# Kernel optimization log

Measured on AMD Instinct MI355X. Metric: run time of the kernel, lower is better.

## Reference

```python
import jax, jax.numpy as jnp
import numpy as np

D = 2048      # input_dim
E = 64        # num_experts
K = 2         # top-k
TEMP = 1.0    # temperature


def setup_inputs() -> dict:
    key = jax.random.key(0)
    ks = jax.random.split(key, 10)
    B, S = 4, 4096
    x = jax.random.normal(ks[0], (B, S, D), dtype=jnp.float32)
    u = jax.random.uniform(ks[1], (B, S, E), dtype=jnp.float32, minval=1e-7, maxval=1.0 - 1e-7)
    # Xavier-uniform init like the torch module (bias zeros)
    def xavier(k, fan_in, fan_out):
        lim = np.sqrt(6.0 / (fan_in + fan_out))
        return jax.random.uniform(k, (fan_in, fan_out), dtype=jnp.float32, minval=-lim, maxval=lim)
    return {
        "x": x, "u": u,
        "W1r": xavier(ks[2], D, D), "b1r": jnp.zeros((D,), jnp.float32),
        "W2r": xavier(ks[3], D, E), "b2r": jnp.zeros((E,), jnp.float32),
        "W1b": xavier(ks[4], D, D), "b1b": jnp.zeros((D,), jnp.float32),
        "W2b": xavier(ks[5], D, 1), "b2b": jnp.zeros((1,), jnp.float32),
    }


def reference(x, u, W1r, b1r, W2r, b2r, W1b, b1b, W2b, b2b):
    # Router MLP: Linear -> GELU(exact) -> Linear  (dropout=0)
    h_r = jax.nn.gelu(jnp.einsum("bsd,de->bse", x, W1r) + b1r, approximate=False)
    expert_scores = jnp.einsum("bsd,de->bse", h_r, W2r) + b2r            # [B,S,E]
    # Baseline MLP -> scalar per token
    h_b = jax.nn.gelu(jnp.einsum("bsd,de->bse", x, W1b) + b1b, approximate=False)
    baseline = (jnp.einsum("bsd,de->bse", h_b, W2b) + b2b)[..., 0]       # [B,S]
    # Training path: Gumbel noise + softmax + top-k (first softmax in torch src is dead code)
    gumbel = -jnp.log(-jnp.log(u))
    expert_probs = jax.nn.softmax((expert_scores + gumbel) / TEMP, axis=-1)
    expert_weights, expert_indices = jax.lax.top_k(expert_probs, K)      # [B,S,K]
    policy_gradient = jax.lax.stop_gradient(expert_weights - baseline[..., None])
    return expert_weights, expert_indices, baseline, policy_gradient, expert_scores
```

## Files before the change

### kernel.cpp

```cpp
#include <hip/hip_runtime.h>
#include <math.h>

#define D_IN   2048
#define E_NUM  64
#define NTOK   16384

#define BM     64
#define BN     256
#define BK     32
#define NTHR   256
#define LDA    68
#define LDH    68
#define NCHUNK (D_IN / BN)
#define NKITER (D_IN / BK)


__global__ __launch_bounds__(NTHR, 2)
void fused_mlp_kernel(const float* __restrict__ x,
                      const float* __restrict__ W1r, const float* __restrict__ b1r,
                      const float* __restrict__ W2r, const float* __restrict__ b2r,
                      const float* __restrict__ W1b, const float* __restrict__ b1b,
                      const float* __restrict__ W2b, const float* __restrict__ b2b,
                      float* __restrict__ out_scores,
                      float* __restrict__ out_baseline)
{
    extern __shared__ float smem[];
    float* As  = smem;
    float* Bs  = smem + BK * LDA;
    float* hsT = smem;

    const int tid    = threadIdx.x;
    const int isBase = blockIdx.y;
    const int row0   = blockIdx.x * BM;

    const float* W1 = isBase ? W1b : W1r;
    const float* b1 = isBase ? b1b : b1r;

    const int ty = tid >> 5;
    const int tx = tid & 31;

    const int sm  = tid >> 3;
    const int skq = tid & 7;
    const int bk4 = tid >> 6;
    const int bn4 = (tid & 63) * 4;

    const int sy = tid >> 4;
    const int sx = tid & 15;
    double acc2[4][4] = {};
    const int tb = tid & 63;
    const int hg = tid >> 6;
    double blacc = 0.0;

    for (int ch = 0; ch < NCHUNK; ++ch) {
        const int col0 = ch * BN;
        double acc[8][8] = {};

        for (int kc = 0; kc < NKITER; ++kc) {
            const int k0 = kc * BK;
            __syncthreads();

            const float* xp = x + (size_t)(row0 + sm) * D_IN + (k0 + 4 * skq);
            float4 xv0 = *(const float4*)xp;
            float4 xv1 = *(const float4*)(xp + (size_t)32 * D_IN);
            const float* wp = W1 + (size_t)(k0 + bk4) * D_IN + (col0 + bn4);
            float4 wv[8];
            #pragma unroll
            for (int j = 0; j < 8; ++j)
                wv[j] = *(const float4*)(wp + (size_t)(4 * j) * D_IN);

            As[(4 * skq + 0) * LDA + sm] = xv0.x;
            As[(4 * skq + 1) * LDA + sm] = xv0.y;
            As[(4 * skq + 2) * LDA + sm] = xv0.z;
            As[(4 * skq + 3) * LDA + sm] = xv0.w;
            As[(4 * skq + 0) * LDA + sm + 32] = xv1.x;
            As[(4 * skq + 1) * LDA + sm + 32] = xv1.y;
            As[(4 * skq + 2) * LDA + sm + 32] = xv1.z;
            As[(4 * skq + 3) * LDA + sm + 32] = xv1.w;
            #pragma unroll
            for (int j = 0; j < 8; ++j)
                *(float4*)&Bs[(bk4 + 4 * j) * BN + bn4] = wv[j];

            __syncthreads();

            #pragma unroll 4
            for (int kk = 0; kk < BK; ++kk) {
                float4 A0 = *(float4*)&As[kk * LDA + 8 * ty];
                float4 A1 = *(float4*)&As[kk * LDA + 8 * ty + 4];
                float4 B0 = *(float4*)&Bs[kk * BN + 4 * tx];
                float4 B1 = *(float4*)&Bs[kk * BN + 128 + 4 * tx];
                double a64[8] = {(double)A0.x, (double)A0.y, (double)A0.z, (double)A0.w,
                                 (double)A1.x, (double)A1.y, (double)A1.z, (double)A1.w};
                double b64[8] = {(double)B0.x, (double)B0.y, (double)B0.z, (double)B0.w,
                                 (double)B1.x, (double)B1.y, (double)B1.z, (double)B1.w};
                #pragma unroll
                for (int i = 0; i < 8; ++i)
                    #pragma unroll
                    for (int j = 0; j < 8; ++j)
                        acc[i][j] = fma(a64[i], b64[j], acc[i][j]);
            }
        }

        __syncthreads();
        #pragma unroll
        for (int j = 0; j < 8; ++j) {
            const int c = (j < 4) ? (4 * tx + j) : (128 + 4 * tx + (j - 4));
            const double bias = (double)b1[col0 + c];
            float h[8];
            #pragma unroll
            for (int i = 0; i < 8; ++i) {
                const double z = acc[i][j] + bias;
                h[i] = (float)(0.5 * z * (1.0 + erf(z * 0.70710678118654752440)));
            }
            *(float4*)&hsT[c * LDH + 8 * ty]     = make_float4(h[0], h[1], h[2], h[3]);
            *(float4*)&hsT[c * LDH + 8 * ty + 4] = make_float4(h[4], h[5], h[6], h[7]);
        }
        __syncthreads();

        if (!isBase) {
            #pragma unroll 2
            for (int hq = 0; hq < BN / 4; ++hq) {
                #pragma unroll
                for (int s = 0; s < 4; ++s) {
                    const int h = 4 * hq + s;
                    float4 A  = *(float4*)&hsT[h * LDH + 4 * sy];
                    float4 Bv = *(const float4*)&W2r[(size_t)(col0 + h) * E_NUM + 4 * sx];
                    double av[4] = {(double)A.x, (double)A.y, (double)A.z, (double)A.w};
                    double bv[4] = {(double)Bv.x, (double)Bv.y, (double)Bv.z, (double)Bv.w};
                    #pragma unroll
                    for (int r = 0; r < 4; ++r)
                        #pragma unroll
                        for (int e = 0; e < 4; ++e)
                            acc2[r][e] = fma(av[r], bv[e], acc2[r][e]);
                }
            }
        } else {
            #pragma unroll 4
            for (int hh = 0; hh < 64; ++hh) {
                const int h = hg * 64 + hh;
                blacc = fma((double)hsT[h * LDH + tb], (double)W2b[col0 + h], blacc);
            }
        }
    }

    __syncthreads();

    if (!isBase) {
        #pragma unroll
        for (int r = 0; r < 4; ++r) {
            float4 o;
            o.x = (float)(acc2[r][0] + (double)b2r[4 * sx + 0]);
            o.y = (float)(acc2[r][1] + (double)b2r[4 * sx + 1]);
            o.z = (float)(acc2[r][2] + (double)b2r[4 * sx + 2]);
            o.w = (float)(acc2[r][3] + (double)b2r[4 * sx + 3]);
            *(float4*)&out_scores[(size_t)(row0 + 4 * sy + r) * E_NUM + 4 * sx] = o;
        }
    } else {
        double* red = (double*)smem;
        red[tid] = blacc;
        __syncthreads();
        if (tid < 64) {
            double bl = red[tid] + red[64 + tid] + red[128 + tid] + red[192 + tid]
                      + (double)b2b[0];
            out_baseline[row0 + tid] = (float)bl;
        }
    }
}

__global__ __launch_bounds__(256)
void softmax_topk_kernel(const float* __restrict__ scores,
                         const float* __restrict__ u,
                         const float* __restrict__ baseline,
                         float* __restrict__ out_w,
                         float* __restrict__ out_i,
                         float* __restrict__ out_pg)
{
    const int tok  = (blockIdx.x * blockDim.x + threadIdx.x) >> 6;
    const int lane = threadIdx.x & 63;

    const double s  = (double)scores[(size_t)tok * E_NUM + lane];
    const double uu = (double)u[(size_t)tok * E_NUM + lane];
    const double g  = -log(-log(uu));
    const double v  = s + g;

    double m = v;
    #pragma unroll
    for (int off = 32; off > 0; off >>= 1)
        m = fmax(m, __shfl_xor(m, off, 64));
    const double p = exp(v - m);
    double sum = p;
    #pragma unroll
    for (int off = 32; off > 0; off >>= 1)
        sum += __shfl_xor(sum, off, 64);
    const float w = (float)(p / sum);

    float w1 = w; int i1 = lane;
    #pragma unroll
    for (int off = 32; off > 0; off >>= 1) {
        const float ov = __shfl_xor(w1, off, 64);
        const int   oi = __shfl_xor(i1, off, 64);
        if (ov > w1 || (ov == w1 && oi < i1)) { w1 = ov; i1 = oi; }
    }
    float w2 = (lane == i1) ? -1.0f : w; int i2 = lane;
    #pragma unroll
    for (int off = 32; off > 0; off >>= 1) {
        const float ov = __shfl_xor(w2, off, 64);
        const int   oi = __shfl_xor(i2, off, 64);
        if (ov > w2 || (ov == w2 && oi < i2)) { w2 = ov; i2 = oi; }
    }

    if (lane == 0) {
        const float bl = baseline[tok];
        out_w [(size_t)tok * 2 + 0] = w1;
        out_w [(size_t)tok * 2 + 1] = w2;
        out_i [(size_t)tok * 2 + 0] = (float)i1;
        out_i [(size_t)tok * 2 + 1] = (float)i2;
        out_pg[(size_t)tok * 2 + 0] = w1 - bl;
        out_pg[(size_t)tok * 2 + 1] = w2 - bl;
    }
}

extern "C" void kernel_launch(void* const* d_in, const int* in_sizes, int n_in,
                              void* d_out, int out_size, void* d_ws, size_t ws_size,
                              hipStream_t stream) {
    const float* x   = (const float*)d_in[0];
    const float* u   = (const float*)d_in[1];
    const float* W1r = (const float*)d_in[2];
    const float* b1r = (const float*)d_in[3];
    const float* W2r = (const float*)d_in[4];
    const float* b2r = (const float*)d_in[5];
    const float* W1b = (const float*)d_in[6];
    const float* b1b = (const float*)d_in[7];
    const float* W2b = (const float*)d_in[8];
    const float* b2b = (const float*)d_in[9];

    float* out     = (float*)d_out;
    float* out_w   = out;
    float* out_i   = out + 32768;
    float* out_bl  = out + 65536;
    float* out_pg  = out + 81920;
    float* out_sc  = out + 114688;

    const size_t smem_bytes = (size_t)BN * LDH * sizeof(float);

    dim3 g1(NTOK / BM, 2);
    fused_mlp_kernel<<<g1, NTHR, smem_bytes, stream>>>(
        x, W1r, b1r, W2r, b2r, W1b, b1b, W2b, b2b, out_sc, out_bl);

    softmax_topk_kernel<<<dim3((NTOK * 64) / 256), 256, 0, stream>>>(
        out_sc, u, out_bl, out_w, out_i, out_pg);
}
```

Before: 6.922 ms.

## Double-buffer shared-memory tiles with register prefetch in first-layer GEMM

Restructures the first-layer GEMM main loop to use two shared-memory buffers with BK halved to 16. Global loads for tile k+2 are issued into registers while tile k is computed, and tile k+1 is stored to the alternate buffer. This cuts the main loop to one barrier per iteration and hides global load latency behind the FP64 FMA work. In exchange it adds register pressure and shared-memory footprint, and the smaller K tile means more loop iterations.

```diff
diff --git a/kernel.cpp b/kernel.cpp
--- a/kernel.cpp
+++ b/kernel.cpp
@@ -7,12 +7,18 @@
 
 #define BM     64
 #define BN     256
-#define BK     32
+#define BK2    16
 #define NTHR   256
 #define LDA    68
+#define BSL    256
 #define LDH    68
 #define NCHUNK (D_IN / BN)
-#define NKITER (D_IN / BK)
+#define NK2    (D_IN / BK2)
+
+#define AS0_OFF 0
+#define BS0_OFF 1088
+#define AS1_OFF 5184
+#define BS1_OFF 6272
 
 
 __global__ __launch_bounds__(NTHR, 2)
@@ -25,8 +31,6 @@
                       float* __restrict__ out_baseline)
 {
     extern __shared__ float smem[];
-    float* As  = smem;
-    float* Bs  = smem + BK * LDA;
     float* hsT = smem;
 
     const int tid    = threadIdx.x;
@@ -39,10 +43,10 @@
     const int ty = tid >> 5;
     const int tx = tid & 31;
 
-    const int sm  = tid >> 3;
-    const int skq = tid & 7;
-    const int bk4 = tid >> 6;
-    const int bn4 = (tid & 63) * 4;
+    const int sm2  = tid >> 2;
+    const int skq2 = tid & 3;
+    const int bk   = tid >> 6;
+    const int bn4  = (tid & 63) * 4;
 
     const int sy = tid >> 4;
     const int sx = tid & 15;
@@ -51,43 +55,78 @@
     const int hg = tid >> 6;
     double blacc = 0.0;
 
+    const float* xrow = x + (size_t)(row0 + sm2) * D_IN + 4 * skq2;
+
     for (int ch = 0; ch < NCHUNK; ++ch) {
         const int col0 = ch * BN;
         double acc[8][8] = {};
 
-        for (int kc = 0; kc < NKITER; ++kc) {
-            const int k0 = kc * BK;
+        __syncthreads();
+
+        float4 xv = *(const float4*)(xrow + 0);
+        float4 wv0, wv1, wv2, wv3;
+        {
+            const float* wp = W1 + (size_t)(0 + bk) * D_IN + (col0 + bn4);
+            wv0 = *(const float4*)(wp + (size_t)0 * D_IN);
+            wv1 = *(const float4*)(wp + (size_t)4 * D_IN);
+            wv2 = *(const float4*)(wp + (size_t)8 * D_IN);
+            wv3 = *(const float4*)(wp + (size_t)12 * D_IN);
+        }
+        {
+            float* As = smem + AS0_OFF;
+            float* Bs = smem + BS0_OFF;
+            As[(4 * skq2 + 0) * LDA + sm2] = xv.x;
+            As[(4 * skq2 + 1) * LDA + sm2] = xv.y;
+            As[(4 * skq2 + 2) * LDA + sm2] = xv.z;
+            As[(4 * skq2 + 3) * LDA + sm2] = xv.w;
+            *(float4*)&Bs[(bk + 0)  * BSL + bn4] = wv0;
+            *(float4*)&Bs[(bk + 4)  * BSL + bn4] = wv1;
+            *(float4*)&Bs[(bk + 8)  * BSL + bn4] = wv2;
+            *(float4*)&Bs[(bk + 12) * BSL + bn4] = wv3;
+        }
+        xv = *(const float4*)(xrow + BK2);
+        {
+            const float* wp = W1 + (size_t)(BK2 + bk) * D_IN + (col0 + bn4);
+            wv0 = *(const float4*)(wp + (size_t)0 * D_IN);
+            wv1 = *(const float4*)(wp + (size_t)4 * D_IN);
+            wv2 = *(const float4*)(wp + (size_t)8 * D_IN);
+            wv3 = *(const float4*)(wp + (size_t)12 * D_IN);
+        }
+
+        for (int kc = 0; kc < NK2; ++kc) {
+            float* Asc = smem + ((kc & 1) ? AS1_OFF : AS0_OFF);
+            float* Bsc = smem + ((kc & 1) ? BS1_OFF : BS0_OFF);
+            float* Asn = smem + ((kc & 1) ? AS0_OFF : AS1_OFF);
+            float* Bsn = smem + ((kc & 1) ? BS0_OFF : BS1_OFF);
+
             __syncthreads();
 
-            const float* xp = x + (size_t)(row0 + sm) * D_IN + (k0 + 4 * skq);
-            float4 xv0 = *(const float4*)xp;
-            float4 xv1 = *(const float4*)(xp + (size_t)32 * D_IN);
-            const float* wp = W1 + (size_t)(k0 + bk4) * D_IN + (col0 + bn4);
-            float4 wv[8];
-            #pragma unroll
-            for (int j = 0; j < 8; ++j)
-                wv[j] = *(const float4*)(wp + (size_t)(4 * j) * D_IN);
-
-            As[(4 * skq + 0) * LDA + sm] = xv0.x;
-            As[(4 * skq + 1) * LDA + sm] = xv0.y;
-            As[(4 * skq + 2) * LDA + sm] = xv0.z;
-            As[(4 * skq + 3) * LDA + sm] = xv0.w;
-            As[(4 * skq + 0) * LDA + sm + 32] = xv1.x;
-            As[(4 * skq + 1) * LDA + sm + 32] = xv1.y;
-            As[(4 * skq + 2) * LDA + sm + 32] = xv1.z;
-            As[(4 * skq + 3) * LDA + sm + 32] = xv1.w;
-            #pragma unroll
-            for (int j = 0; j < 8; ++j)
-                *(float4*)&Bs[(bk4 + 4 * j) * BN + bn4] = wv[j];
-
-            __syncthreads();
-
-            #pragma unroll 4
-            for (int kk = 0; kk < BK; ++kk) {
-                float4 A0 = *(float4*)&As[kk * LDA + 8 * ty];
-                float4 A1 = *(float4*)&As[kk * LDA + 8 * ty + 4];
-                float4 B0 = *(float4*)&Bs[kk * BN + 4 * tx];
-                float4 B1 = *(float4*)&Bs[kk * BN + 128 + 4 * tx];
+            if (kc < NK2 - 1) {
+                Asn[(4 * skq2 + 0) * LDA + sm2] = xv.x;
+                Asn[(4 * skq2 + 1) * LDA + sm2] = xv.y;
+                Asn[(4 * skq2 + 2) * LDA + sm2] = xv.z;
+                Asn[(4 * skq2 + 3) * LDA + sm2] = xv.w;
+                *(float4*)&Bsn[(bk + 0)  * BSL + bn4] = wv0;
+                *(float4*)&Bsn[(bk + 4)  * BSL + bn4] = wv1;
+                *(float4*)&Bsn[(bk + 8)  * BSL + bn4] = wv2;
+                *(float4*)&Bsn[(bk + 12) * BSL + bn4] = wv3;
+                if (kc < NK2 - 2) {
+                    const int k0n = (kc + 2) * BK2;
+                    xv = *(const float4*)(xrow + k0n);
+                    const float* wp = W1 + (size_t)(k0n + bk) * D_IN + (col0 + bn4);
+                    wv0 = *(const float4*)(wp + (size_t)0 * D_IN);
+                    wv1 = *(const float4*)(wp + (size_t)4 * D_IN);
+                    wv2 = *(const float4*)(wp + (size_t)8 * D_IN);
+                    wv3 = *(const float4*)(wp + (size_t)12 * D_IN);
+                }
+            }
+
+            #pragma unroll 8
+            for (int kk = 0; kk < BK2; ++kk) {
+                float4 A0 = *(float4*)&Asc[kk * LDA + 8 * ty];
+                float4 A1 = *(float4*)&Asc[kk * LDA + 8 * ty + 4];
+                float4 B0 = *(float4*)&Bsc[kk * BSL + 4 * tx];
+                float4 B1 = *(float4*)&Bsc[kk * BSL + 128 + 4 * tx];
                 double a64[8] = {(double)A0.x, (double)A0.y, (double)A0.z, (double)A0.w,
                                  (double)A1.x, (double)A1.y, (double)A1.z, (double)A1.w};
                 double b64[8] = {(double)B0.x, (double)B0.y, (double)B0.z, (double)B0.w,
```

Measured after the change: 6.351 ms. 1.09x faster.
